# Optimization experiments

Hardware: AMD Instinct MI355X
Metric: run time of the kernel (lower is better)

## Reference

```python
import jax, jax.numpy as jnp
import numpy as np
from jax import lax

DIM = 1024
INNER = 2048          # expansion * dim
GROUPS = 128          # groups in cell's 1x1 grouped convs
GSZ = INNER // GROUPS # 16
KSZ = 4               # causal conv kernel size
EPS = 1e-8


def log_g(x):
    return jnp.where(x >= 0, jnp.log(jax.nn.relu(x) + 0.5 + EPS), -jax.nn.softplus(-x) + EPS)


def setup_inputs() -> dict:
    key = jax.random.key(0)
    ks = jax.random.split(key, 10)
    B, S = 4, 4096
    std_up = float(np.sqrt(2.0 / (5 * DIM)))
    std_down = float(2.0 / 1 / np.sqrt(DIM))
    return {
        "x": jax.random.normal(ks[0], (B, S, DIM), jnp.float32),
        "w_up": jax.random.normal(ks[1], (2 * INNER, DIM), jnp.float32) * std_up,
        "b_up": jnp.zeros((2 * INNER,), jnp.float32),
        "conv_w": jax.random.normal(ks[2], (INNER, 1, KSZ), jnp.float32) * 0.25,
        "conv_b": jnp.zeros((INNER,), jnp.float32),
        "skip": jnp.ones((INNER,), jnp.float32),
        "w_f": jax.random.normal(ks[3], (GROUPS, GSZ, GSZ), jnp.float32) * 0.1,
        "w_i": jax.random.normal(ks[4], (GROUPS, GSZ, GSZ), jnp.float32) * 0.1,
        "w_h": jax.random.normal(ks[5], (GROUPS, GSZ, GSZ), jnp.float32) * 0.1,
        "w_down": jax.random.normal(ks[6], (DIM, INNER), jnp.float32) * std_down,
        "b_down": jnp.zeros((DIM,), jnp.float32),
    }


def reference(x, w_up, b_up, conv_w, conv_b, skip, w_f, w_i, w_h, w_down, b_down):
    B, S, _ = x.shape
    # proj up -> split into minlstm branch and gate branch z
    x_inner = jnp.einsum('bsd,ed->bse', x, w_up) + b_up          # (B,S,2*INNER)
    x_min, z = jnp.split(x_inner, 2, axis=-1)                    # each (B,S,INNER)

    # causal depthwise conv over time (left pad K-1, cross-correlation like torch)
    xc = lax.conv_general_dilated(
        x_min.transpose(0, 2, 1), conv_w,
        window_strides=(1,), padding=[(KSZ - 1, 0)],
        feature_group_count=INNER,
        dimension_numbers=('NCH', 'OIH', 'NCH'))
    xc = (xc + conv_b[None, :, None]).transpose(0, 2, 1)         # (B,S,INNER)
    act = jax.nn.silu(xc)

    # minLSTM cell: grouped (block-diagonal, 128 blocks of 16) 1x1 projections
    ag = act.reshape(B, S, GROUPS, GSZ)
    f_gate = jnp.einsum('bsgi,goi->bsgo', ag, w_f).reshape(B, S, INNER)
    i_gate = jnp.einsum('bsgi,goi->bsgo', ag, w_i).reshape(B, S, INNER)
    hidden = jnp.einsum('bsgi,goi->bsgo', ag, w_h).reshape(B, S, INNER)

    diff = jax.nn.softplus(-f_gate) - jax.nn.softplus(-i_gate)
    log_f = -jax.nn.softplus(diff)
    log_i = -jax.nn.softplus(-diff)
    log_tilde_h = log_g(hidden)

    # parallel log-space scan
    a_star = jnp.cumsum(log_f + EPS, axis=1)
    log_h0_b = lax.cumlogsumexp(log_i + log_tilde_h - a_star, axis=1)
    h_t = jnp.exp(a_star + log_h0_b)                             # (B,S,INNER)

    # original code keeps only last timestep of the scan, broadcast over skip path
    h = h_t[:, -1:, :] + skip * act                              # (B,S,INNER)
    h = h * jax.nn.silu(z)
    out = jnp.einsum('bse,de->bsd', h, w_down) + b_down          # (B,S,DIM)
    return out
```

## Files before the change

### kernel.cpp

```cpp
#include <hip/hip_runtime.h>
#include <math.h>

constexpr int B_  = 4;
constexpr int S_  = 4096;
constexpr int D_  = 1024;
constexpr int IN_ = 2048;
constexpr float EPS_ = 1e-8f;
constexpr int NCH_ = 128;
constexpr int CS_  = S_ / NCH_;
constexpr float LOG2E_ = 1.4426950408889634f;
constexpr float LN2_   = 0.6931471805599453f;
constexpr float EPS2_  = 1.4426950408889634e-8f;

typedef __attribute__((ext_vector_type(8))) _Float16 f16x8;
typedef __attribute__((ext_vector_type(2))) _Float16 h2;
typedef __attribute__((ext_vector_type(4))) float    f32x4;

#define BAR() asm volatile("s_barrier" ::: "memory")

__device__ __forceinline__ h2 pkrtz(float a, float b) {
  auto r = __builtin_amdgcn_cvt_pkrtz(a, b);
  union { decltype(r) r_; h2 h; } c; c.r_ = r; return c.h;
}
__device__ __forceinline__ unsigned packh2(float a, float b) {
  auto r = __builtin_amdgcn_cvt_pkrtz(a, b);
  union { decltype(r) r_; unsigned u; } c; c.r_ = r; return c.u;
}
__device__ __forceinline__ void unpack_h8(uint4 v, float* f) {
  union { uint4 u; _Float16 h[8]; } c; c.u = v;
  #pragma unroll
  for (int i = 0; i < 8; ++i) f[i] = (float)c.h[i];
}
__device__ __forceinline__ float sp2(float t) {
  const float e = __builtin_amdgcn_exp2f(-fabsf(t));
  return fmaxf(t, 0.0f) + __builtin_amdgcn_logf(1.0f + e);
}
__device__ __forceinline__ float siluf(float x) {
  return x * __builtin_amdgcn_rcpf(1.0f + __builtin_amdgcn_exp2f(-x * LOG2E_));
}

__device__ __forceinline__ void gload16(const void* g, void* l) {
  __builtin_amdgcn_global_load_lds(
      (const __attribute__((address_space(1))) void*)g,
      (__attribute__((address_space(3))) void*)l,
      16, 0, 0);
}

__launch_bounds__(256)
__global__ void cvt_f16_2(const float* __restrict__ in0, unsigned* __restrict__ out0,
                          long n8_0,
                          const float* __restrict__ in1, unsigned* __restrict__ out1,
                          long n8_1)
{
  const long total  = n8_0 + n8_1;
  const long stride = (long)gridDim.x * blockDim.x;
  for (long t = (long)blockIdx.x * blockDim.x + threadIdx.x; t < total; t += stride) {
    const float* in  = (t < n8_0) ? in0  : in1;
    unsigned*    out = (t < n8_0) ? out0 : out1;
    const long   i   = (t < n8_0) ? t    : t - n8_0;
    const float4 a = *(const float4*)(in + i * 8);
    const float4 b = *(const float4*)(in + i * 8 + 4);
    uint4 o;
    o.x = packh2(a.x, a.y);
    o.y = packh2(a.z, a.w);
    o.z = packh2(b.x, b.y);
    o.w = packh2(b.z, b.w);
    *(uint4*)(out + i * 4) = o;
  }
}

__launch_bounds__(256)
__global__ void cvt_f16(const float* __restrict__ in, unsigned* __restrict__ outp,
                        long n8)
{
  const long stride = (long)gridDim.x * blockDim.x;
  for (long i = (long)blockIdx.x * blockDim.x + threadIdx.x; i < n8; i += stride) {
    const float4 a = *(const float4*)(in + i * 8);
    const float4 b = *(const float4*)(in + i * 8 + 4);
    uint4 o;
    o.x = packh2(a.x, a.y);
    o.y = packh2(a.z, a.w);
    o.z = packh2(b.x, b.y);
    o.w = packh2(b.z, b.w);
    *(uint4*)(outp + i * 4) = o;
  }
}

template<int MODE>
__launch_bounds__(512, 4)
__global__ void gemm_mfma(const unsigned short* __restrict__ Ab,
                          const unsigned short* __restrict__ Bb,
                          const float* __restrict__ bias,
                          void* __restrict__ out0,
                          unsigned short* __restrict__ out1,
                          int M, int N, int K)
{
  constexpr int BM = 128, BN = 256, BK = 32;
  __shared__ __align__(16) unsigned short Ls[3 * BM * BK + 3 * BN * BK];

  const int tid  = threadIdx.x;
  const int lane = tid & 63;
  const int w    = tid >> 6;
  const int wm   = w >> 2;
  const int wn   = w & 3;

  const int GX  = gridDim.x;
  const int nwg = GX * gridDim.y;
  int lin = blockIdx.y * GX + blockIdx.x;
  lin = (lin & 7) * (nwg >> 3) + (lin >> 3);
  const int m0 = (lin / GX) * BM;
  const int n0 = (lin % GX) * BN;
  const int NT = K / BK;

  const int sr2  = lane >> 2;
  const int sblk = ((lane & 3) ^ ((lane >> 3) & 3)) * 8;

  const int fr  = lane & 15;
  const int fcb = (((lane >> 4) ^ ((lane >> 1) & 3))) * 8;

  auto stageA = [&](int buf, int kOff) {
    gload16(Ab + (size_t)(m0 + w * 16 + sr2) * K + kOff + sblk,
            &Ls[buf * (BM * BK) + (w * 16) * BK]);
  };
  auto stageB = [&](int buf, int kOff) {
    gload16(Bb + (size_t)(n0 + w * 16 + sr2) * K + kOff + sblk,
            &Ls[3 * BM * BK + buf * (BN * BK) + (w * 16) * BK]);
    gload16(Bb + (size_t)(n0 + 128 + w * 16 + sr2) * K + kOff + sblk,
            &Ls[3 * BM * BK + buf * (BN * BK) + (128 + w * 16) * BK]);
  };

  f32x4 acc[4][4] = {};

  stageA(0, 0);  stageB(0, 0);
  stageA(1, BK); stageB(1, BK);
  asm volatile("s_waitcnt vmcnt(3)" ::: "memory");
  BAR();

  int bufc = 0;
  for (int t = 0; t < NT; ++t) {
    const unsigned short* AL = &Ls[bufc * (BM * BK)];
    const unsigned short* BL = &Ls[3 * BM * BK + bufc * (BN * BK)];
    const int bufn = (bufc + 2 >= 3) ? bufc - 1 : bufc + 2;

    if (t + 2 < NT) {
      stageA(bufn, (t + 2) * BK);
      stageB(bufn, (t + 2) * BK);
    }

    f16x8 af[4], bf[4];
    #pragma unroll
    for (int i = 0; i < 4; ++i)
      af[i] = *(const f16x8*)&AL[(wm * 64 + i * 16 + fr) * BK + fcb];
    #pragma unroll
    for (int j = 0; j < 4; ++j)
      bf[j] = *(const f16x8*)&BL[(wn * 64 + j * 16 + fr) * BK + fcb];

    BAR();
    __builtin_amdgcn_s_setprio(1);
    #pragma unroll
    for (int i = 0; i < 4; ++i)
      #pragma unroll
      for (int j = 0; j < 4; ++j)
        acc[i][j] = __builtin_amdgcn_mfma_f32_16x16x32_f16(af[i], bf[j], acc[i][j], 0, 0, 0);
    __builtin_amdgcn_s_setprio(0);
    if (t + 2 < NT) asm volatile("s_waitcnt vmcnt(3)" ::: "memory");
    else            asm volatile("s_waitcnt vmcnt(0)" ::: "memory");
    BAR();
    bufc = (bufc + 1 >= 3) ? 0 : bufc + 1;
  }

  const int col = lane & 15;
  const int rb4 = (lane >> 4) * 4;

  if (MODE == 1) {
    #pragma unroll
    for (int j = 0; j < 4; ++j) {
      const int n  = n0 + wn * 64 + j * 16 + col;
      const float bv = bias[n];
      #pragma unroll
      for (int i = 0; i < 4; ++i) {
        const int mb = m0 + wm * 64 + i * 16 + rb4;
        #pragma unroll
        for (int r = 0; r < 4; ++r)
          ((float*)out0)[(size_t)(mb + r) * N + n] = acc[i][j][r] + bv;
      }
    }
  } else {
    BAR();
    constexpr int RS = 72;
    unsigned short* eb = Ls + w * (32 * RS);
    const bool zhalf = (n0 >= IN_);
    float bv[4];
    #pragma unroll
    for (int j = 0; j < 4; ++j) bv[j] = bias[n0 + wn * 64 + j * 16 + col];

    const int lrow = lane >> 3;
    const int lc8  = (lane & 7) * 8;
    unsigned short* dst = zhalf ? out1 : (unsigned short*)out0;
    const int ncol0 = (zhalf ? n0 - IN_ : n0) + wn * 64 + lc8;

    #pragma unroll
    for (int p = 0; p < 2; ++p) {
      asm volatile("s_waitcnt lgkmcnt(0)" ::: "memory");
      #pragma unroll
      for (int i2 = 0; i2 < 2; ++i2)
        #pragma unroll
        for (int j = 0; j < 4; ++j)
          #pragma unroll
          for (int r = 0; r < 4; ++r) {
            const float v = acc[p * 2 + i2][j][r] + bv[j];
            ((_Float16*)eb)[(i2 * 16 + rb4 + r) * RS + j * 16 + col] = (_Float16)v;
          }
      asm volatile("s_waitcnt lgkmcnt(0)" ::: "memory");
      #pragma unroll
      for (int it = 0; it < 4; ++it) {
        const int row = it * 8 + lrow;
        uint4 d = *(const uint4*)&eb[row * RS + lc8];
        if (zhalf) {
          float f[8];
          unpack_h8(d, f);
          d.x = packh2(siluf(f[0]), siluf(f[1]));
          d.y = packh2(siluf(f[2]), siluf(f[3]));
          d.z = packh2(siluf(f[4]), siluf(f[5]));
          d.w = packh2(siluf(f[6]), siluf(f[7]));
        }
        const int m = m0 + wm * 64 + p * 32 + row;
        *(uint4*)(dst + (size_t)m * IN_ + ncol0) = d;
      }
    }
  }
}

__launch_bounds__(256)
__global__ void conv_silu_k(const uint4* __restrict__ xm,
                            const float* __restrict__ cw,
                            const float* __restrict__ cb,
                            uint4* __restrict__ act)
{
  const int t = blockIdx.x * 256 + threadIdx.x;
  const int c8 = t & 255;
  const int s4 = (t >> 8) & (S_ / 4 - 1);
  const int b  = t >> 18;
  const int c  = c8 * 8;
  constexpr int RW = IN_ / 8;

  float w[8][4];
  #pragma unroll
  for (int j = 0; j < 8; ++j)
    *(float4*)w[j] = *(const float4*)(cw + (size_t)(c + j) * 4);
  float bias8[8];
  *(float4*)(bias8)     = *(const float4*)(cb + c);
  *(float4*)(bias8 + 4) = *(const float4*)(cb + c + 4);

  const size_t rowb = ((size_t)b * S_ + s4 * 4) * RW + c8;
  float xf[7][8];
  #pragma unroll
  for (int i = 0; i < 7; ++i) {
    if (s4 == 0 && i < 3) {
      #pragma unroll
      for (int j = 0; j < 8; ++j) xf[i][j] = 0.0f;
    } else {
      unpack_h8(xm[rowb + (long)(i - 3) * RW], xf[i]);
    }
  }

  #pragma unroll
  for (int o = 0; o < 4; ++o) {
    float r[8];
    #pragma unroll
    for (int j = 0; j < 8; ++j) r[j] = bias8[j];
    #pragma unroll
    for (int k = 0; k < 4; ++k)
      #pragma unroll
      for (int j = 0; j < 8; ++j)
        r[j] = fmaf(xf[o + k][j], w[j][k], r[j]);
    uint4 ov;
    ov.x = packh2(siluf(r[0]), siluf(r[1]));
    ov.y = packh2(siluf(r[2]), siluf(r[3]));
    ov.z = packh2(siluf(r[4]), siluf(r[5]));
    ov.w = packh2(siluf(r[6]), siluf(r[7]));
    act[rowb + (size_t)o * RW] = ov;
  }
}

__launch_bounds__(256)
__global__ void gates_scan(const unsigned* __restrict__ actb,
                           const float* __restrict__ wf,
                           const float* __restrict__ wi,
                           const float* __restrict__ wh,
                           float2* __restrict__ part)
{
  const int T  = blockIdx.x * 256 + threadIdx.x;
  const int o  = T & 15;
  const int g  = (T >> 4) & 127;
  const int ck = (T >> 11) & (NCH_ - 1);
  const int b  = T >> 18;

  h2 Wf2[8], Wi2[8], Wh2[8];
  const float* pf = wf + ((size_t)g * 16 + o) * 16;
  const float* pi = wi + ((size_t)g * 16 + o) * 16;
  const float* ph = wh + ((size_t)g * 16 + o) * 16;
  #pragma unroll
  for (int i = 0; i < 8; ++i) {
    Wf2[i] = pkrtz(pf[2 * i] * LOG2E_, pf[2 * i + 1] * LOG2E_);
    Wi2[i] = pkrtz(pi[2 * i] * LOG2E_, pi[2 * i + 1] * LOG2E_);
    Wh2[i] = pkrtz(ph[2 * i], ph[2 * i + 1]);
  }

  float p = 0.0f, Mx = -INFINITY, Ss = 0.0f;
  const unsigned* ap = actb + ((size_t)b * S_ + (size_t)ck * CS_) * (IN_ / 2) + g * 8;
  for (int s = 0; s < CS_; ++s) {
    union { uint4 u; h2 h[4]; } A0, A1;
    A0.u = *(const uint4*)(ap);
    A1.u = *(const uint4*)(ap + 4);
    ap += IN_ / 2;
    float fg = 0.0f, ig = 0.0f, hd = 0.0f;
    #pragma unroll
    for (int i = 0; i < 4; ++i) {
      fg = __builtin_amdgcn_fdot2(A0.h[i], Wf2[i], fg, false);
      ig = __builtin_amdgcn_fdot2(A0.h[i], Wi2[i], ig, false);
      hd = __builtin_amdgcn_fdot2(A0.h[i], Wh2[i], hd, false);
    }
    #pragma unroll
    for (int i = 0; i < 4; ++i) {
      fg = __builtin_amdgcn_fdot2(A1.h[i], Wf2[i + 4], fg, false);
      ig = __builtin_amdgcn_fdot2(A1.h[i], Wi2[i + 4], ig, false);
      hd = __builtin_amdgcn_fdot2(A1.h[i], Wh2[i + 4], hd, false);
    }
    const float diff  = sp2(-fg) - sp2(-ig);
    const float log_f = -sp2(diff);
    const float log_i = diff + log_f;
    const float lpos  = __builtin_amdgcn_logf(hd + 0.5f + EPS_);
    const float lneg  = -sp2(-hd * LOG2E_) + EPS2_;
    const float log_th = (hd >= 0.0f) ? lpos : lneg;
    p += log_f + EPS2_;
    const float v = log_i + log_th - p;
    const float m = fmaxf(Mx, v);
    Ss = Ss * __builtin_amdgcn_exp2f(Mx - m) + __builtin_amdgcn_exp2f(v - m);
    Mx = m;
  }
  part[((size_t)(b * IN_ + g * 16 + o)) * NCH_ + ck] =
      make_float2(p, Mx + __builtin_amdgcn_logf(Ss));
}

__launch_bounds__(256)
__global__ void combine_k(const float2* __restrict__ part, float* __restrict__ hlast)
{
  const int seq = blockIdx.x * 256 + threadIdx.x;
  if (seq >= B_ * IN_) return;
  const float2* pp = part + (size_t)seq * NCH_;
  float P = 0.0f, Mx = -INFINITY, Ss = 0.0f;
  for (int c = 0; c < NCH_; ++c) {
    const float2 al = pp[c];
    const float v = al.y - P;
    const float m = fmaxf(Mx, v);
    Ss = Ss * __builtin_amdgcn_exp2f(Mx - m) + __builtin_amdgcn_exp2f(v - m);
    Mx = m;
    P += al.x;
  }
  hlast[seq] = __builtin_amdgcn_exp2f(P + Mx) * Ss;
}

__launch_bounds__(256)
__global__ void gfuse_k(const unsigned* __restrict__ actb,
                        unsigned* __restrict__ zb,
                        const float* __restrict__ hlast,
                        const float* __restrict__ skipv)
{
  const size_t total  = (size_t)B_ * S_ * IN_ / 8;
  const size_t stride = (size_t)gridDim.x * blockDim.x;
  for (size_t t = (size_t)blockIdx.x * blockDim.x + threadIdx.x; t < total; t += stride) {
    const size_t e = t * 8;
    const int    c = (int)(e % IN_);
    const int    b = (int)(e / ((size_t)S_ * IN_));
    float a[8], z[8], hl[8], sk[8];
    unpack_h8(*(const uint4*)(actb + e / 2), a);
    unpack_h8(*(const uint4*)(zb   + e / 2), z);
    *(float4*)(hl)     = *(const float4*)(hlast + (size_t)b * IN_ + c);
    *(float4*)(hl + 4) = *(const float4*)(hlast + (size_t)b * IN_ + c + 4);
    *(float4*)(sk)     = *(const float4*)(skipv + c);
    *(float4*)(sk + 4) = *(const float4*)(skipv + c + 4);
    float g[8];
    #pragma unroll
    for (int j = 0; j < 8; ++j) g[j] = (hl[j] + sk[j] * a[j]) * z[j];
    uint4 o;
    o.x = packh2(g[0], g[1]);
    o.y = packh2(g[2], g[3]);
    o.z = packh2(g[4], g[5]);
    o.w = packh2(g[6], g[7]);
    *(uint4*)(zb + e / 2) = o;
  }
}

extern "C" void kernel_launch(void* const* d_in, const int* in_sizes, int n_in,
                              void* d_out, int out_size, void* d_ws, size_t ws_size,
                              hipStream_t stream)
{
  const float* x     = (const float*)d_in[0];
  const float* w_up  = (const float*)d_in[1];
  const float* b_up  = (const float*)d_in[2];
  const float* cw    = (const float*)d_in[3];
  const float* cb    = (const float*)d_in[4];
  const float* skipv = (const float*)d_in[5];
  const float* w_f   = (const float*)d_in[6];
  const float* w_i   = (const float*)d_in[7];
  const float* w_h   = (const float*)d_in[8];
  const float* w_dn  = (const float*)d_in[9];
  const float* b_dn  = (const float*)d_in[10];
  float* out = (float*)d_out;

  char* ws = (char*)d_ws;
  unsigned short* xminb = (unsigned short*)(ws);
  unsigned short* wdb   = (unsigned short*)(ws);
  float2*         part  = (float2*)(ws + 8388608ULL);
  float*          hlast = (float*)(ws + 16777216ULL);
  unsigned short* zb    = (unsigned short*)(ws + 67108864ULL);
  unsigned short* actb  = (unsigned short*)(ws + 134217728ULL);
  unsigned short* xb    = (unsigned short*)(ws + 134217728ULL);
  unsigned short* wub   = (unsigned short*)(ws + 201326592ULL);

  const int M = B_ * S_;

  cvt_f16_2<<<2560, 256, 0, stream>>>(
      x,    (unsigned*)xb,  (long)M * D_ / 8,
      w_up, (unsigned*)wub, (long)2 * IN_ * D_ / 8);

  gemm_mfma<0><<<dim3((2 * IN_) / 256, M / 128), 512, 0, stream>>>(
      xb, wub, b_up, xminb, (unsigned short*)zb, M, 2 * IN_, D_);

  conv_silu_k<<<(B_ * (S_ / 4) * (IN_ / 8)) / 256, 256, 0, stream>>>(
      (const uint4*)xminb, cw, cb, (uint4*)actb);

  cvt_f16<<<256, 256, 0, stream>>>(w_dn, (unsigned*)wdb, (long)D_ * IN_ / 8);

  gates_scan<<<(B_ * 128 * 16 * NCH_) / 256, 256, 0, stream>>>(
      (const unsigned*)actb, w_f, w_i, w_h, part);

  combine_k<<<(B_ * IN_ + 255) / 256, 256, 0, stream>>>(part, hlast);

  gfuse_k<<<2048, 256, 0, stream>>>((const unsigned*)actb, (unsigned*)zb, hlast, skipv);

  gemm_mfma<1><<<dim3(D_ / 256, M / 128), 512, 0, stream>>>(
      zb, wdb, b_dn, out, nullptr, M, D_, IN_);
}
```

Baseline: 420.5 us.

## Pre-pack weights into MFMA fragment layout and load B directly from global

```diff
diff --git a/kernel.cpp b/kernel.cpp
--- a/kernel.cpp
+++ b/kernel.cpp
@@ -9,7 +9,6 @@
 constexpr int NCH_ = 128;
 constexpr int CS_  = S_ / NCH_;
 constexpr float LOG2E_ = 1.4426950408889634f;
-constexpr float LN2_   = 0.6931471805599453f;
 constexpr float EPS2_  = 1.4426950408889634e-8f;
 
 typedef __attribute__((ext_vector_type(8))) _Float16 f16x8;
@@ -44,29 +43,6 @@
       (const __attribute__((address_space(1))) void*)g,
       (__attribute__((address_space(3))) void*)l,
       16, 0, 0);
-}
-
-__launch_bounds__(256)
-__global__ void cvt_f16_2(const float* __restrict__ in0, unsigned* __restrict__ out0,
-                          long n8_0,
-                          const float* __restrict__ in1, unsigned* __restrict__ out1,
-                          long n8_1)
-{
-  const long total  = n8_0 + n8_1;
-  const long stride = (long)gridDim.x * blockDim.x;
-  for (long t = (long)blockIdx.x * blockDim.x + threadIdx.x; t < total; t += stride) {
-    const float* in  = (t < n8_0) ? in0  : in1;
-    unsigned*    out = (t < n8_0) ? out0 : out1;
-    const long   i   = (t < n8_0) ? t    : t - n8_0;
-    const float4 a = *(const float4*)(in + i * 8);
-    const float4 b = *(const float4*)(in + i * 8 + 4);
-    uint4 o;
-    o.x = packh2(a.x, a.y);
-    o.y = packh2(a.z, a.w);
-    o.z = packh2(b.x, b.y);
-    o.w = packh2(b.z, b.w);
-    *(uint4*)(out + i * 4) = o;
-  }
 }
 
 __launch_bounds__(256)
@@ -86,17 +62,37 @@
   }
 }
 
+__launch_bounds__(256)
+__global__ void pack_b(const float* __restrict__ w, uint4* __restrict__ bp, int K)
+{
+  const int t    = blockIdx.x * 256 + threadIdx.x;
+  const int l    = t & 63;
+  const int tile = t >> 6;
+  const int KT   = K >> 5;
+  const int nt   = tile / KT;
+  const int kt   = tile - nt * KT;
+  const float* src = w + (size_t)(nt * 16 + (l & 15)) * K + kt * 32 + ((l >> 4) << 3);
+  const float4 a = *(const float4*)src;
+  const float4 b = *(const float4*)(src + 4);
+  uint4 o;
+  o.x = packh2(a.x, a.y);
+  o.y = packh2(a.z, a.w);
+  o.z = packh2(b.x, b.y);
+  o.w = packh2(b.z, b.w);
+  bp[t] = o;
+}
+
 template<int MODE>
 __launch_bounds__(512, 4)
-__global__ void gemm_mfma(const unsigned short* __restrict__ Ab,
-                          const unsigned short* __restrict__ Bb,
-                          const float* __restrict__ bias,
-                          void* __restrict__ out0,
-                          unsigned short* __restrict__ out1,
-                          int M, int N, int K)
-{
-  constexpr int BM = 128, BN = 256, BK = 32;
-  __shared__ __align__(16) unsigned short Ls[3 * BM * BK + 3 * BN * BK];
+__global__ void gemm_bl2(const unsigned short* __restrict__ Ab,
+                         const unsigned short* __restrict__ Bp,
+                         const float* __restrict__ bias,
+                         void* __restrict__ out0,
+                         unsigned short* __restrict__ out1,
+                         int M, int N, int K)
+{
+  constexpr int BM = 128, BN = 256, BK = 64;
+  __shared__ __align__(16) unsigned short Ls[3 * BM * BK];
 
   const int tid  = threadIdx.x;
   const int lane = tid & 63;
@@ -105,66 +101,80 @@
   const int wn   = w & 3;
 
   const int GX  = gridDim.x;
-  const int nwg = GX * gridDim.y;
-  int lin = blockIdx.y * GX + blockIdx.x;
-  lin = (lin & 7) * (nwg >> 3) + (lin >> 3);
-  const int m0 = (lin / GX) * BM;
-  const int n0 = (lin % GX) * BN;
+  const int CR  = gridDim.y >> 3;
+  const int BW  = (GX < 8) ? GX : 8;
+  const int orig = blockIdx.y * GX + blockIdx.x;
+  const int xcd = orig & 7, cl = orig >> 3;
+  const int band = cl / (CR * BW);
+  const int rr   = cl - band * (CR * BW);
+  const int yl   = rr / BW;
+  const int xin  = rr - yl * BW;
+  const int m0 = (xcd * CR + yl) * BM;
+  const int n0 = (band * BW + xin) * BN;
   const int NT = K / BK;
-
-  const int sr2  = lane >> 2;
-  const int sblk = ((lane & 3) ^ ((lane >> 3) & 3)) * 8;
+  const int KT = K >> 5;
+
+  const int sr   = lane >> 3;
+  const int sblk = ((lane & 7) ^ sr) * 8;
+  auto stageA = [&](int buf, int kOff) {
+    gload16(Ab + (size_t)(m0 + w * 16 + sr) * K + kOff + sblk,
+            &Ls[buf * (BM * BK) + (w * 16) * BK]);
+    gload16(Ab + (size_t)(m0 + w * 16 + 8 + sr) * K + kOff + sblk,
+            &Ls[buf * (BM * BK) + (w * 16 + 8) * BK]);
+  };
 
   const int fr  = lane & 15;
-  const int fcb = (((lane >> 4) ^ ((lane >> 1) & 3))) * 8;
-
-  auto stageA = [&](int buf, int kOff) {
-    gload16(Ab + (size_t)(m0 + w * 16 + sr2) * K + kOff + sblk,
-            &Ls[buf * (BM * BK) + (w * 16) * BK]);
-  };
-  auto stageB = [&](int buf, int kOff) {
-    gload16(Bb + (size_t)(n0 + w * 16 + sr2) * K + kOff + sblk,
-            &Ls[3 * BM * BK + buf * (BN * BK) + (w * 16) * BK]);
-    gload16(Bb + (size_t)(n0 + 128 + w * 16 + sr2) * K + kOff + sblk,
-            &Ls[3 * BM * BK + buf * (BN * BK) + (128 + w * 16) * BK]);
-  };
+  const int fb0 = (((lane >> 4) + 0) ^ (lane & 7)) * 8;
+  const int fb1 = (((lane >> 4) + 4) ^ (lane & 7)) * 8;
+
+  const f16x8* Bpv = (const f16x8*)Bp;
+  const int ntb = (n0 >> 4) + wn * 4;
 
   f32x4 acc[4][4] = {};
 
-  stageA(0, 0);  stageB(0, 0);
-  stageA(1, BK); stageB(1, BK);
-  asm volatile("s_waitcnt vmcnt(3)" ::: "memory");
+  stageA(0, 0); stageA(1, BK);
+  asm volatile("s_waitcnt vmcnt(2)" ::: "memory");
   BAR();
 
   int bufc = 0;
   for (int t = 0; t < NT; ++t) {
     const unsigned short* AL = &Ls[bufc * (BM * BK)];
-    const unsigned short* BL = &Ls[3 * BM * BK + bufc * (BN * BK)];
-    const int bufn = (bufc + 2 >= 3) ? bufc - 1 : bufc + 2;
-
-    if (t + 2 < NT) {
-      stageA(bufn, (t + 2) * BK);
-      stageB(bufn, (t + 2) * BK);
-    }
-
-    f16x8 af[4], bf[4];
+    const int  bufn = (bufc + 2 >= 3) ? bufc - 1 : bufc + 2;
+    const bool more = (t + 2 < NT);
+
+    f16x8 bf[4][2];
+    #pragma unroll
+    for (int j = 0; j < 4; ++j) {
+      bf[j][0] = Bpv[((size_t)(ntb + j) * KT + 2 * t) * 64 + lane];
+      bf[j][1] = Bpv[((size_t)(ntb + j) * KT + 2 * t + 1) * 64 + lane];
+    }
+    if (more) stageA(bufn, (t + 2) * BK);
+
+    f16x8 af[4];
     #pragma unroll
     for (int i = 0; i < 4; ++i)
-      af[i] = *(const f16x8*)&AL[(wm * 64 + i * 16 + fr) * BK + fcb];
-    #pragma unroll
-    for (int j = 0; j < 4; ++j)
-      bf[j] = *(const f16x8*)&BL[(wn * 64 + j * 16 + fr) * BK + fcb];
+      af[i] = *(const f16x8*)&AL[(wm * 64 + i * 16 + fr) * BK + fb0];
 
     BAR();
+    if (more) asm volatile("s_waitcnt vmcnt(2)" ::: "memory");
+    else      asm volatile("s_waitcnt vmcnt(0)" ::: "memory");
     __builtin_amdgcn_s_setprio(1);
     #pragma unroll
     for (int i = 0; i < 4; ++i)
       #pragma unroll
       for (int j = 0; j < 4; ++j)
-        acc[i][j] = __builtin_amdgcn_mfma_f32_16x16x32_f16(af[i], bf[j], acc[i][j], 0, 0, 0);
+        acc[i][j] = __builtin_amdgcn_mfma_f32_16x16x32_f16(af[i], bf[j][0], acc[i][j], 0, 0, 0);
     __builtin_amdgcn_s_setprio(0);
-    if (t + 2 < NT) asm volatile("s_waitcnt vmcnt(3)" ::: "memory");
-    else            asm volatile("s_waitcnt vmcnt(0)" ::: "memory");
+    #pragma unroll
+    for (int i = 0; i < 4; ++i)
+      af[i] = *(const f16x8*)&AL[(wm * 64 + i * 16 + fr) * BK + fb1];
+    __builtin_amdgcn_s_setprio(1);
+    #pragma unroll
+    for (int i = 0; i < 4; ++i)
+      #pragma unroll
+      for (int j = 0; j < 4; ++j)
+        acc[i][j] = __builtin_amdgcn_mfma_f32_16x16x32_f16(af[i], bf[j][1], acc[i][j], 0, 0, 0);
+    __builtin_amdgcn_s_setprio(0);
     BAR();
     bufc = (bufc + 1 >= 3) ? 0 : bufc + 1;
   }
@@ -411,27 +421,27 @@
 
   char* ws = (char*)d_ws;
   unsigned short* xminb = (unsigned short*)(ws);
-  unsigned short* wdb   = (unsigned short*)(ws);
+  uint4*          bpd   = (uint4*)(ws);
   float2*         part  = (float2*)(ws + 8388608ULL);
   float*          hlast = (float*)(ws + 16777216ULL);
   unsigned short* zb    = (unsigned short*)(ws + 67108864ULL);
   unsigned short* actb  = (unsigned short*)(ws + 134217728ULL);
   unsigned short* xb    = (unsigned short*)(ws + 134217728ULL);
-  unsigned short* wub   = (unsigned short*)(ws + 201326592ULL);
+  uint4*          bpu   = (uint4*)(ws + 201326592ULL);
 
   const int M = B_ * S_;
 
-  cvt_f16_2<<<2560, 256, 0, stream>>>(
-      x,    (unsigned*)xb,  (long)M * D_ / 8,
-      w_up, (unsigned*)wub, (long)2 * IN_ * D_ / 8);
-
-  gemm_mfma<0><<<dim3((2 * IN_) / 256, M / 128), 512, 0, stream>>>(
-      xb, wub, b_up, xminb, (unsigned short*)zb, M, 2 * IN_, D_);
+  cvt_f16<<<2048, 256, 0, stream>>>(x, (unsigned*)xb, (long)M * D_ / 8);
+  pack_b<<<(2 * IN_ * D_ / 8) / 256, 256, 0, stream>>>(w_up, bpu, D_);
+
+  gemm_bl2<0><<<dim3((2 * IN_) / 256, M / 128), 512, 0, stream>>>(
+      xb, (const unsigned short*)bpu, b_up, xminb, (unsigned short*)zb,
+      M, 2 * IN_, D_);
 
   conv_silu_k<<<(B_ * (S_ / 4) * (IN_ / 8)) / 256, 256, 0, stream>>>(
       (const uint4*)xminb, cw, cb, (uint4*)actb);
 
-  cvt_f16<<<256, 256, 0, stream>>>(w_dn, (unsigned*)wdb, (long)D_ * IN_ / 8);
+  pack_b<<<(D_ * IN_ / 8) / 256, 256, 0, stream>>>(w_dn, bpd, IN_);
 
   gates_scan<<<(B_ * 128 * 16 * NCH_) / 256, 256, 0, stream>>>(
       (const unsigned*)actb, w_f, w_i, w_h, part);
@@ -440,6 +450,6 @@
 
   gfuse_k<<<2048, 256, 0, stream>>>((const unsigned*)actb, (unsigned*)zb, hlast, skipv);
 
-  gemm_mfma<1><<<dim3(D_ / 256, M / 128), 512, 0, stream>>>(
-      zb, wdb, b_dn, out, nullptr, M, D_, IN_);
-}
+  gemm_bl2<1><<<dim3(D_ / 256, M / 128), 512, 0, stream>>>(
+      zb, (const unsigned short*)bpd, b_dn, out, nullptr, M, D_, IN_);
+}
```

New measurement: 414.9 us. Within noise of the previous version (-1.3%).
